# Optimization experiments

Hardware: AMD Instinct MI355X
Metric: run time of the kernel (lower is better)

## Reference

```python
import jax, jax.numpy as jnp
import numpy as np


def setup_inputs() -> dict:
    key = jax.random.key(0)
    k = jax.random.split(key, 4)
    B, F, E, U = 4096, 40, 64, 64
    return {
        "x": jax.random.normal(k[0], (B, F, E), dtype=jnp.float32),
        "attention_W": jax.random.normal(k[1], (E, U), dtype=jnp.float32) * (2.0 / (E + U)) ** 0.5,
        "attention_b": jnp.zeros((U,), dtype=jnp.float32),
        "projection_h": jax.random.normal(k[2], (U, 1), dtype=jnp.float32) * (2.0 / (U + 1)) ** 0.5,
        "projection_p": jax.random.normal(k[3], (E, 1), dtype=jnp.float32) * (2.0 / (E + 1)) ** 0.5,
    }


def reference(x, attention_W, attention_b, projection_h, projection_p):
    # x: [B, F, E] stacked field embeddings (original code takes a list of F [B,1,E])
    F = x.shape[1]
    ri, ci = np.triu_indices(F, k=1)  # static pair indices, P = F*(F-1)/2
    inner_product = x[:, ri, :] * x[:, ci, :]            # [B, P, E]
    attention_tmp = jax.nn.relu(
        jnp.einsum('bpe,eu->bpu', inner_product, attention_W) + attention_b
    )                                                    # [B, P, U]
    scores = jnp.einsum('bpu,uo->bpo', attention_tmp, projection_h)  # [B, P, 1]
    attention_weight = jax.nn.softmax(scores, axis=1)    # softmax over pairs
    attention_output = jnp.sum(inner_product * attention_weight, axis=1)  # [B, E]
    # dropout omitted (inference / eval mode)
    afm_out = attention_output @ projection_p            # [B, 1]
    return afm_out
```

## Files before the change

kernel.cpp:

```cpp
#include <hip/hip_runtime.h>
#include <hip/hip_fp16.h>

typedef _Float16 half8v __attribute__((ext_vector_type(8)));
typedef _Float16 half2v __attribute__((ext_vector_type(2)));
typedef float f32x4 __attribute__((ext_vector_type(4)));

#define DPP_XADD(x, ctrl)                                                          \
  x += __builtin_bit_cast(float, __builtin_amdgcn_mov_dpp(                         \
           __builtin_bit_cast(int, x), ctrl, 0xf, 0xf, true))

__global__ void afm_prep(const float* __restrict__ W, const float* __restrict__ pvec,
                         unsigned char* __restrict__ ws) {
  const int tid = threadIdx.x;
  _Float16* wf = (_Float16*)ws;
  _Float16* pf = (_Float16*)(ws + 8192);
  unsigned int* tbl = (unsigned int*)(ws + 10240);
  for (int idx = tid; idx < 4096; idx += 256) {
    int j = idx & 7, lane = (idx >> 3) & 63, nt = (idx >> 9) & 3, ks = idx >> 11;
    int k = ks * 32 + (lane >> 4) * 8 + j;
    int u = nt * 16 + (lane & 15);
    wf[idx] = (_Float16)W[k * 64 + u];
  }
  for (int idx = tid; idx < 1024; idx += 256) {
    int j = idx & 7, lane = (idx >> 3) & 63, ks = idx >> 9;
    int k = ks * 32 + (lane >> 4) * 8 + j;
    pf[idx] = ((lane & 15) == 0) ? (_Float16)pvec[k] : (_Float16)0.f;
  }
  for (int p = tid; p < 784; p += 256) {
    int pc = p > 779 ? 779 : p;
    int i = 0, rem = pc;
    while (rem >= 39 - i) { rem -= 39 - i; ++i; }
    int j = i + 1 + rem;
    tbl[p] = ((unsigned)(i * 72) << 16) | (unsigned)(j * 72);
  }
}

#define ISSUE_READS(slot, offw)                                                    \
  do {                                                                             \
    const _Float16* xi_ = &xh[((offw) >> 16) + eoff];                              \
    const _Float16* xj_ = &xh[((offw) & 0xffffu) + eoff];                          \
    xia[slot][0] = *(const half8v*)xi_;                                            \
    xia[slot][1] = *(const half8v*)(xi_ + 32);                                     \
    xja[slot][0] = *(const half8v*)xj_;                                            \
    xja[slot][1] = *(const half8v*)(xj_ + 32);                                     \
  } while (0)

__global__ __launch_bounds__(256) void afm_main(
    const float* __restrict__ x, const float* __restrict__ bvec,
    const float* __restrict__ hvec, const unsigned char* __restrict__ ws,
    float* __restrict__ out) {
  __shared__ __align__(16) _Float16 xh[40 * 72];
  __shared__ float scs[784];
  __shared__ float s2s[784];
  __shared__ float red[12];

  const int tid = threadIdx.x;
  const int b = blockIdx.x;
  const int lane = tid & 63;
  const int wid = tid >> 6;
  const int m = lane & 15, kg = lane >> 4;

  const float4* xg = (const float4*)(x + b * 2560);
  float4 v0 = xg[tid];
  float4 v1 = xg[256 + tid];
  float4 v2;
  if (tid < 128) v2 = xg[512 + tid];

  const unsigned int* tbl_g = (const unsigned int*)(ws + 10240);
  unsigned int off[13];
#pragma unroll
  for (int i = 0; i < 13; ++i) {
    int tt = wid + 4 * i;
    tt = tt > 48 ? 48 : tt;
    off[i] = tbl_g[16 * tt + m];
  }

  const half8v* wfg = (const half8v*)ws;
  half8v wf[2][4];
#pragma unroll
  for (int ks = 0; ks < 2; ++ks)
#pragma unroll
    for (int nt = 0; nt < 4; ++nt) wf[ks][nt] = wfg[(ks * 4 + nt) * 64 + lane];
  const half8v* pfg = (const half8v*)(ws + 8192);
  half8v pf[2] = {pfg[lane], pfg[64 + lane]};
  float bu[4], hu[4];
#pragma unroll
  for (int nt = 0; nt < 4; ++nt) {
    int uu = nt * 16 + m;
    bu[nt] = bvec[uu];
    hu[nt] = hvec[uu];
  }

  {
    int f = tid >> 4, e4 = tid & 15;
    half2v* dst = (half2v*)&xh[f * 72 + e4 * 4];
    dst[0] = __builtin_bit_cast(half2v, __builtin_amdgcn_cvt_pkrtz(v0.x, v0.y));
    dst[1] = __builtin_bit_cast(half2v, __builtin_amdgcn_cvt_pkrtz(v0.z, v0.w));
  }
  {
    int g = 256 + tid;
    int f = g >> 4, e4 = g & 15;
    half2v* dst = (half2v*)&xh[f * 72 + e4 * 4];
    dst[0] = __builtin_bit_cast(half2v, __builtin_amdgcn_cvt_pkrtz(v1.x, v1.y));
    dst[1] = __builtin_bit_cast(half2v, __builtin_amdgcn_cvt_pkrtz(v1.z, v1.w));
  }
  if (tid < 128) {
    int g = 512 + tid;
    int f = g >> 4, e4 = g & 15;
    half2v* dst = (half2v*)&xh[f * 72 + e4 * 4];
    dst[0] = __builtin_bit_cast(half2v, __builtin_amdgcn_cvt_pkrtz(v2.x, v2.y));
    dst[1] = __builtin_bit_cast(half2v, __builtin_amdgcn_cvt_pkrtz(v2.z, v2.w));
  }
  __syncthreads();

  const int eoff = kg * 8;
  half8v xia[2][2], xja[2][2];
  ISSUE_READS(0, off[0]);
#pragma unroll
  for (int i = 0; i < 13; ++i) {
    const int cur = i & 1;
    if (i < 12) ISSUE_READS(cur ^ 1, off[i + 1]);
    half8v a0 = xia[cur][0] * xja[cur][0];
    half8v a1 = xia[cur][1] * xja[cur][1];
    f32x4 acc[4];
#pragma unroll
    for (int nt = 0; nt < 4; ++nt) {
      acc[nt] = (f32x4){bu[nt], bu[nt], bu[nt], bu[nt]};
      acc[nt] = __builtin_amdgcn_mfma_f32_16x16x32_f16(a0, wf[0][nt], acc[nt], 0, 0, 0);
      acc[nt] = __builtin_amdgcn_mfma_f32_16x16x32_f16(a1, wf[1][nt], acc[nt], 0, 0, 0);
    }
    f32x4 accp = (f32x4){0.f, 0.f, 0.f, 0.f};
    accp = __builtin_amdgcn_mfma_f32_16x16x32_f16(a0, pf[0], accp, 0, 0, 0);
    accp = __builtin_amdgcn_mfma_f32_16x16x32_f16(a1, pf[1], accp, 0, 0, 0);

    int tt = wid + 4 * i;
    tt = tt > 48 ? 48 : tt;
    const int t16 = 16 * tt;
#pragma unroll
    for (int r = 0; r < 4; ++r) {
      float s = fmaxf(acc[0][r], 0.f) * hu[0] + fmaxf(acc[1][r], 0.f) * hu[1] +
                fmaxf(acc[2][r], 0.f) * hu[2] + fmaxf(acc[3][r], 0.f) * hu[3];
      DPP_XADD(s, 0xB1);
      DPP_XADD(s, 0x4E);
      DPP_XADD(s, 0x141);
      DPP_XADD(s, 0x140);
      int pr = t16 + kg * 4 + r;
      if (m == 0 && pr < 780) {
        scs[pr] = s;
        s2s[pr] = accp[r];
      }
    }
  }
  __syncthreads();

  float sv[4];
  float mx = -1e30f;
#pragma unroll
  for (int k2 = 0; k2 < 4; ++k2) {
    int p = tid + k2 * 256;
    if (p < 780) {
      sv[k2] = scs[p];
      mx = fmaxf(mx, sv[k2]);
    } else {
      sv[k2] = -1e30f;
    }
  }
#pragma unroll
  for (int o = 32; o; o >>= 1) mx = fmaxf(mx, __shfl_xor(mx, o));
  if (lane == 0) red[wid] = mx;
  __syncthreads();
  mx = fmaxf(fmaxf(red[0], red[1]), fmaxf(red[2], red[3]));
  float num = 0.f, den = 0.f;
#pragma unroll
  for (int k2 = 0; k2 < 4; ++k2) {
    int p = tid + k2 * 256;
    if (p < 780) {
      float e = __expf(sv[k2] - mx);
      num += e * s2s[p];
      den += e;
    }
  }
#pragma unroll
  for (int o = 32; o; o >>= 1) {
    num += __shfl_xor(num, o);
    den += __shfl_xor(den, o);
  }
  if (lane == 0) { red[4 + wid] = num; red[8 + wid] = den; }
  __syncthreads();
  if (tid == 0)
    out[b] = (red[4] + red[5] + red[6] + red[7]) /
             (red[8] + red[9] + red[10] + red[11]);
}

extern "C" void kernel_launch(void* const* d_in, const int* in_sizes, int n_in,
                              void* d_out, int out_size, void* d_ws, size_t ws_size,
                              hipStream_t stream) {
  const float* x    = (const float*)d_in[0];
  const float* W    = (const float*)d_in[1];
  const float* bvec = (const float*)d_in[2];
  const float* hvec = (const float*)d_in[3];
  const float* pvec = (const float*)d_in[4];
  float* out = (float*)d_out;
  unsigned char* ws = (unsigned char*)d_ws;

  hipLaunchKernelGGL(afm_prep, dim3(1), dim3(256), 0, stream, W, pvec, ws);
  hipLaunchKernelGGL(afm_main, dim3(4096), dim3(256), 0, stream,
                     x, bvec, hvec, ws, out);
}
```

Measured before the change: 136.9 us.

## Transpose MFMA operands so score reduction is per-lane and stage pair table in LDS

Swaps the A/B operands of the MFMAs so each lane holds the four U-values for one pair. The score reduction then becomes per-lane FMAs plus two cross-row shuffles, replacing four DPP adds per output row. The bias is loaded as a vector accumulator init. The pair-offset table now goes into shared memory once, and offsets are read from LDS two iterations ahead, instead of holding 13 global loads in registers. This is meant to cut register pressure and the per-row reduction work, at the cost of an extra LDS array and LDS reads inside the loop.

```diff
diff --git a/kernel.cpp b/kernel.cpp
--- a/kernel.cpp
+++ b/kernel.cpp
@@ -4,10 +4,6 @@
 typedef _Float16 half8v __attribute__((ext_vector_type(8)));
 typedef _Float16 half2v __attribute__((ext_vector_type(2)));
 typedef float f32x4 __attribute__((ext_vector_type(4)));
-
-#define DPP_XADD(x, ctrl)                                                          \
-  x += __builtin_bit_cast(float, __builtin_amdgcn_mov_dpp(                         \
-           __builtin_bit_cast(int, x), ctrl, 0xf, 0xf, true))
 
 __global__ void afm_prep(const float* __restrict__ W, const float* __restrict__ pvec,
                          unsigned char* __restrict__ ws) {
@@ -50,6 +46,7 @@
     const float* __restrict__ hvec, const unsigned char* __restrict__ ws,
     float* __restrict__ out) {
   __shared__ __align__(16) _Float16 xh[40 * 72];
+  __shared__ __align__(16) unsigned int tblu[784];
   __shared__ float scs[784];
   __shared__ float s2s[784];
   __shared__ float red[12];
@@ -66,13 +63,10 @@
   float4 v2;
   if (tid < 128) v2 = xg[512 + tid];
 
-  const unsigned int* tbl_g = (const unsigned int*)(ws + 10240);
-  unsigned int off[13];
-#pragma unroll
-  for (int i = 0; i < 13; ++i) {
-    int tt = wid + 4 * i;
-    tt = tt > 48 ? 48 : tt;
-    off[i] = tbl_g[16 * tt + m];
+  {
+    const float4* tg = (const float4*)(ws + 10240);
+    float4* ts = (float4*)tblu;
+    if (tid < 196) ts[tid] = tg[tid];
   }
 
   const half8v* wfg = (const half8v*)ws;
@@ -83,12 +77,11 @@
     for (int nt = 0; nt < 4; ++nt) wf[ks][nt] = wfg[(ks * 4 + nt) * 64 + lane];
   const half8v* pfg = (const half8v*)(ws + 8192);
   half8v pf[2] = {pfg[lane], pfg[64 + lane]};
-  float bu[4], hu[4];
+  f32x4 buv[4], huv[4];
 #pragma unroll
   for (int nt = 0; nt < 4; ++nt) {
-    int uu = nt * 16 + m;
-    bu[nt] = bvec[uu];
-    hu[nt] = hvec[uu];
+    buv[nt] = *(const f32x4*)&bvec[nt * 16 + kg * 4];
+    huv[nt] = *(const f32x4*)&hvec[nt * 16 + kg * 4];
   }
 
   {
@@ -114,41 +107,52 @@
   __syncthreads();
 
   const int eoff = kg * 8;
+  const f32x4 zv = (f32x4){0.f, 0.f, 0.f, 0.f};
+  unsigned int off[2];
   half8v xia[2][2], xja[2][2];
+  off[0] = tblu[16 * wid + m];
   ISSUE_READS(0, off[0]);
+  off[1] = tblu[16 * (wid + 4) + m];
 #pragma unroll
   for (int i = 0; i < 13; ++i) {
-    const int cur = i & 1;
-    if (i < 12) ISSUE_READS(cur ^ 1, off[i + 1]);
+    const int cur = i & 1, nxt = cur ^ 1;
+    if (i < 12) ISSUE_READS(nxt, off[nxt]);
+    if (i < 11) {
+      int tn = wid + 4 * (i + 2);
+      tn = tn > 48 ? 48 : tn;
+      off[cur] = tblu[16 * tn + m];
+    }
     half8v a0 = xia[cur][0] * xja[cur][0];
     half8v a1 = xia[cur][1] * xja[cur][1];
     f32x4 acc[4];
 #pragma unroll
     for (int nt = 0; nt < 4; ++nt) {
-      acc[nt] = (f32x4){bu[nt], bu[nt], bu[nt], bu[nt]};
-      acc[nt] = __builtin_amdgcn_mfma_f32_16x16x32_f16(a0, wf[0][nt], acc[nt], 0, 0, 0);
-      acc[nt] = __builtin_amdgcn_mfma_f32_16x16x32_f16(a1, wf[1][nt], acc[nt], 0, 0, 0);
-    }
-    f32x4 accp = (f32x4){0.f, 0.f, 0.f, 0.f};
-    accp = __builtin_amdgcn_mfma_f32_16x16x32_f16(a0, pf[0], accp, 0, 0, 0);
-    accp = __builtin_amdgcn_mfma_f32_16x16x32_f16(a1, pf[1], accp, 0, 0, 0);
+      acc[nt] = __builtin_amdgcn_mfma_f32_16x16x32_f16(wf[0][nt], a0, buv[nt], 0, 0, 0);
+      acc[nt] = __builtin_amdgcn_mfma_f32_16x16x32_f16(wf[1][nt], a1, acc[nt], 0, 0, 0);
+    }
+    f32x4 accp = __builtin_amdgcn_mfma_f32_16x16x32_f16(pf[0], a0, zv, 0, 0, 0);
+    accp = __builtin_amdgcn_mfma_f32_16x16x32_f16(pf[1], a1, accp, 0, 0, 0);
+
+    float sp0 = fmaxf(acc[0][0], 0.f) * huv[0][0];
+    float sp1 = fmaxf(acc[1][0], 0.f) * huv[1][0];
+    float sp2 = fmaxf(acc[2][0], 0.f) * huv[2][0];
+    float sp3 = fmaxf(acc[3][0], 0.f) * huv[3][0];
+#pragma unroll
+    for (int r = 1; r < 4; ++r) {
+      sp0 = fmaf(fmaxf(acc[0][r], 0.f), huv[0][r], sp0);
+      sp1 = fmaf(fmaxf(acc[1][r], 0.f), huv[1][r], sp1);
+      sp2 = fmaf(fmaxf(acc[2][r], 0.f), huv[2][r], sp2);
+      sp3 = fmaf(fmaxf(acc[3][r], 0.f), huv[3][r], sp3);
+    }
+    float s = (sp0 + sp1) + (sp2 + sp3);
+    s += __shfl_xor(s, 16);
+    s += __shfl_xor(s, 32);
 
     int tt = wid + 4 * i;
     tt = tt > 48 ? 48 : tt;
-    const int t16 = 16 * tt;
-#pragma unroll
-    for (int r = 0; r < 4; ++r) {
-      float s = fmaxf(acc[0][r], 0.f) * hu[0] + fmaxf(acc[1][r], 0.f) * hu[1] +
-                fmaxf(acc[2][r], 0.f) * hu[2] + fmaxf(acc[3][r], 0.f) * hu[3];
-      DPP_XADD(s, 0xB1);
-      DPP_XADD(s, 0x4E);
-      DPP_XADD(s, 0x141);
-      DPP_XADD(s, 0x140);
-      int pr = t16 + kg * 4 + r;
-      if (m == 0 && pr < 780) {
-        scs[pr] = s;
-        s2s[pr] = accp[r];
-      }
+    if (kg == 0) {
+      scs[16 * tt + m] = s;
+      s2s[16 * tt + m] = accp[0];
     }
   }
   __syncthreads();
```

After: 129.7 us. 5.2% less time.
